# Optimization experiments

Hardware: AMD Instinct MI355X
Metric: run time of the kernel (lower is better)

## Reference

```python
import jax, jax.numpy as jnp
import numpy as np

# BiDAF-style co-attention with memory_len=2. Dropout is inference-mode identity.

def setup_inputs() -> dict:
    key = jax.random.key(0)
    k1, k2, k3, k4, k5 = jax.random.split(key, 5)
    d = 1024
    inp = jax.random.normal(k1, (8, 4096, d), dtype=jnp.float32)
    mem = jax.random.normal(k2, (8, 2, d), dtype=jnp.float32)
    w_input = jax.random.normal(k3, (d,), dtype=jnp.float32) * (1.0 / np.sqrt(d))
    w_memory = jax.random.normal(k4, (d,), dtype=jnp.float32) * (1.0 / np.sqrt(d))
    dot_scale = jax.random.uniform(k5, (d,), dtype=jnp.float32, minval=0.0, maxval=1.0 / np.sqrt(d))
    return {"input": inp, "memory": mem, "w_input": w_input, "w_memory": w_memory, "dot_scale": dot_scale}


def reference(input, memory, w_input, w_memory, dot_scale):
    # input: [b, L, d]; memory: [b, M=2, d]
    input_dot = jnp.einsum('bld,d->bl', input, w_input)[..., None]        # [b, L, 1]
    memory_dot = jnp.einsum('bmd,d->bm', memory, w_memory)[:, None, :]    # [b, 1, M]
    cross_dot = jnp.einsum('bld,bmd->blm', input * dot_scale, memory)     # [b, L, M]
    att = input_dot + memory_dot + cross_dot                              # [b, L, M]
    weight_one = jax.nn.softmax(att, axis=-1)                             # [b, L, M]
    output_one = jnp.einsum('blm,bmd->bld', weight_one, memory)           # [b, L, d]
    weight_two = jax.nn.softmax(jnp.max(att, axis=-1), axis=-1)           # [b, L]
    output_two = jnp.einsum('bl,bld->bd', weight_two, input)[:, None, :]  # [b, 1, d]
    return jnp.concatenate([input, output_one, input * output_one, output_two * output_one], axis=-1)
```

## Files before the change

### kernel.cpp

```cpp
#include <hip/hip_runtime.h>
#include <stdint.h>


#define BB 8
#define LL 4096
#define DD 1024
#define BPB 128
#define RPB 32
#define RPW 8

__global__ __launch_bounds__(256) void kP(const float* __restrict__ mem,
                                          const float* __restrict__ w_in,
                                          const float* __restrict__ w_mem,
                                          const float* __restrict__ ds,
                                          float* __restrict__ cvec,
                                          float* __restrict__ mdot) {
    int bm = blockIdx.x;
    int t  = threadIdx.x;
    const float* mrow = mem + bm * DD;
    float partial = 0.f;
#pragma unroll
    for (int j = 0; j < 4; ++j) {
        int d = t * 4 + j;
        float m = mrow[d];
        cvec[bm * DD + d] = fmaf(ds[d], m, w_in[d]);
        partial = fmaf(m, w_mem[d], partial);
    }
    __shared__ float red[4];
    for (int off = 32; off; off >>= 1) partial += __shfl_down(partial, off);
    if ((t & 63) == 0) red[t >> 6] = partial;
    __syncthreads();
    if (t == 0) mdot[bm] = red[0] + red[1] + red[2] + red[3];
}

__global__ __launch_bounds__(256) void kA(const float* __restrict__ input,
                                          const float* __restrict__ memory,
                                          const float* __restrict__ cvec,
                                          const float* __restrict__ mdot,
                                          float* __restrict__ att,
                                          float* __restrict__ pmax,
                                          float* __restrict__ pz,
                                          float* __restrict__ pacc,
                                          float* __restrict__ out) {
    int blk = blockIdx.x;
    int b = blk >> 7, chunk = blk & 127;
    int t = threadIdx.x;
    int wave = t >> 6, lane = t & 63;

    const float4* c0p = (const float4*)(cvec + (size_t)b * 2 * DD);
    const float4* c1p = c0p + DD / 4;
    const float4* m0p = (const float4*)(memory + (size_t)b * 2 * DD);
    const float4* m1p = m0p + DD / 4;
    float4 rc0[4], rc1[4], rm0[4], rm1[4], acc[4];
#pragma unroll
    for (int k = 0; k < 4; ++k) {
        rc0[k] = c0p[lane + 64 * k];
        rc1[k] = c1p[lane + 64 * k];
        rm0[k] = m0p[lane + 64 * k];
        rm1[k] = m1p[lane + 64 * k];
        acc[k] = make_float4(0.f, 0.f, 0.f, 0.f);
    }
    float md0 = mdot[b * 2], md1 = mdot[b * 2 + 1];
    float lmax = -1e30f, zsum = 0.f;

    int l0 = chunk * RPB + wave * RPW;
    for (int r = 0; r < RPW; ++r) {
        int l = l0 + r;
        const float4* row = (const float4*)(input + (size_t)(b * LL + l) * DD);
        float4 x[4];
#pragma unroll
        for (int k = 0; k < 4; ++k) x[k] = row[lane + 64 * k];

        float a0 = 0.f, a1 = 0.f;
#pragma unroll
        for (int k = 0; k < 4; ++k) {
            a0 = fmaf(x[k].x, rc0[k].x, a0); a0 = fmaf(x[k].y, rc0[k].y, a0);
            a0 = fmaf(x[k].z, rc0[k].z, a0); a0 = fmaf(x[k].w, rc0[k].w, a0);
            a1 = fmaf(x[k].x, rc1[k].x, a1); a1 = fmaf(x[k].y, rc1[k].y, a1);
            a1 = fmaf(x[k].z, rc1[k].z, a1); a1 = fmaf(x[k].w, rc1[k].w, a1);
        }
        for (int off = 32; off; off >>= 1) {
            a0 += __shfl_xor(a0, off);
            a1 += __shfl_xor(a1, off);
        }
        a0 += md0; a1 += md1;
        if (lane == 0) ((float2*)att)[(size_t)b * LL + l] = make_float2(a0, a1);

        float w0 = 1.f / (1.f + __expf(a1 - a0));
        float w1 = 1.f - w0;
        float ml = fmaxf(a0, a1);

        float e;
        if (ml > lmax) {
            float s = __expf(lmax - ml);
            zsum *= s;
#pragma unroll
            for (int k = 0; k < 4; ++k) {
                acc[k].x *= s; acc[k].y *= s; acc[k].z *= s; acc[k].w *= s;
            }
            lmax = ml;
            e = 1.f;
        } else {
            e = __expf(ml - lmax);
        }
        zsum += e;

        float* orow = out + (size_t)(b * LL + l) * (4 * DD);
#pragma unroll
        for (int k = 0; k < 4; ++k) {
            float4 o1;
            o1.x = fmaf(w0, rm0[k].x, w1 * rm1[k].x);
            o1.y = fmaf(w0, rm0[k].y, w1 * rm1[k].y);
            o1.z = fmaf(w0, rm0[k].z, w1 * rm1[k].z);
            o1.w = fmaf(w0, rm0[k].w, w1 * rm1[k].w);
            ((float4*)orow)[lane + 64 * k] = x[k];
            ((float4*)(orow + DD))[lane + 64 * k] = o1;
            ((float4*)(orow + 2 * DD))[lane + 64 * k] =
                make_float4(x[k].x * o1.x, x[k].y * o1.y,
                            x[k].z * o1.z, x[k].w * o1.w);
            acc[k].x = fmaf(e, x[k].x, acc[k].x);
            acc[k].y = fmaf(e, x[k].y, acc[k].y);
            acc[k].z = fmaf(e, x[k].z, acc[k].z);
            acc[k].w = fmaf(e, x[k].w, acc[k].w);
        }
    }

    __shared__ float swm[4], swz[4];
    __shared__ __align__(16) float sacc[DD];
    if (lane == 0) { swm[wave] = lmax; swz[wave] = zsum; }
    for (int j = t; j < DD; j += 256) sacc[j] = 0.f;
    __syncthreads();
    float bmax = fmaxf(fmaxf(swm[0], swm[1]), fmaxf(swm[2], swm[3]));
    float f = __expf(lmax - bmax);
#pragma unroll
    for (int k = 0; k < 4; ++k) {
        int idx = 4 * (lane + 64 * k);
        atomicAdd(&sacc[idx + 0], f * acc[k].x);
        atomicAdd(&sacc[idx + 1], f * acc[k].y);
        atomicAdd(&sacc[idx + 2], f * acc[k].z);
        atomicAdd(&sacc[idx + 3], f * acc[k].w);
    }
    __syncthreads();
    if (t == 0) {
        float bz = 0.f;
#pragma unroll
        for (int w = 0; w < 4; ++w) bz += swz[w] * __expf(swm[w] - bmax);
        pmax[blk] = bmax;
        pz[blk]   = bz;
    }
    ((float4*)(pacc + (size_t)blk * DD))[t] = ((const float4*)sacc)[t];
}

__global__ __launch_bounds__(256) void kB(const float* __restrict__ pmax,
                                          const float* __restrict__ pz,
                                          const float* __restrict__ pacc,
                                          float* __restrict__ out2) {
    int b = blockIdx.x, t = threadIdx.x;
    __shared__ float se[BPB];
    const float* pm = pmax + b * BPB;
    const float* pzb = pz + b * BPB;
    float m = -1e30f;
    for (int i = 0; i < BPB; ++i) m = fmaxf(m, pm[i]);
    if (t < BPB) se[t] = __expf(pm[t] - m);
    __syncthreads();
    float Z = 0.f;
    for (int i = 0; i < BPB; ++i) Z = fmaf(pzb[i], se[i], Z);
    float invZ = 1.f / Z;

    const float4* P = (const float4*)pacc + (size_t)b * BPB * (DD / 4);
    float4 a = make_float4(0.f, 0.f, 0.f, 0.f);
    for (int i = 0; i < BPB; ++i) {
        float e = se[i];
        float4 v = P[(size_t)i * 256 + t];
        a.x = fmaf(e, v.x, a.x);
        a.y = fmaf(e, v.y, a.y);
        a.z = fmaf(e, v.z, a.z);
        a.w = fmaf(e, v.w, a.w);
    }
    a.x *= invZ; a.y *= invZ; a.z *= invZ; a.w *= invZ;
    ((float4*)(out2 + (size_t)b * DD))[t] = a;
}

__global__ __launch_bounds__(256) void kE(const float* __restrict__ memory,
                                          const float* __restrict__ att,
                                          const float* __restrict__ out2,
                                          float* __restrict__ out) {
    int blk = blockIdx.x;
    int b = blk >> 8, chunk = blk & 255;
    int t = threadIdx.x;
    float4 m0 = ((const float4*)(memory + (size_t)b * 2 * DD))[t];
    float4 m1 = ((const float4*)(memory + (size_t)b * 2 * DD + DD))[t];
    float4 o2 = ((const float4*)(out2 + (size_t)b * DD))[t];
    const float2* attb = (const float2*)att + (size_t)b * LL + chunk * 16;
    for (int r = 0; r < 16; ++r) {
        float2 v = attb[r];
        float w0 = 1.f / (1.f + __expf(v.y - v.x));
        float w1 = 1.f - w0;
        float4 o1;
        o1.x = fmaf(w0, m0.x, w1 * m1.x);
        o1.y = fmaf(w0, m0.y, w1 * m1.y);
        o1.z = fmaf(w0, m0.z, w1 * m1.z);
        o1.w = fmaf(w0, m0.w, w1 * m1.w);
        float* orow = out + (size_t)(b * LL + chunk * 16 + r) * (4 * DD) + 3 * DD;
        ((float4*)orow)[t] = make_float4(o2.x * o1.x, o2.y * o1.y,
                                         o2.z * o1.z, o2.w * o1.w);
    }
}

extern "C" void kernel_launch(void* const* d_in, const int* in_sizes, int n_in,
                              void* d_out, int out_size, void* d_ws, size_t ws_size,
                              hipStream_t stream) {
    const float* input  = (const float*)d_in[0];
    const float* memory = (const float*)d_in[1];
    const float* w_in   = (const float*)d_in[2];
    const float* w_mem  = (const float*)d_in[3];
    const float* ds     = (const float*)d_in[4];
    float* out = (float*)d_out;

    float* ws    = (float*)d_ws;
    float* cvec  = ws;
    float* mdot  = ws + 16384;
    float* att   = ws + 16400;
    float* pmax  = ws + 81936;
    float* pz    = ws + 82960;
    float* out2  = ws + 83984;
    float* pacc  = ws + 92176;

    kP<<<16,   256, 0, stream>>>(memory, w_in, w_mem, ds, cvec, mdot);
    kA<<<1024, 256, 0, stream>>>(input, memory, cvec, mdot, att, pmax, pz, pacc, out);
    kB<<<BB,   256, 0, stream>>>(pmax, pz, pacc, out2);
    kE<<<2048, 256, 0, stream>>>(memory, att, out2, out);
}
```

Measured before the change: 691.6 us.

## Fold prep kernel into main pass, use nontemporal loads/stores, drop LDS atomics

```diff
diff --git a/kernel.cpp b/kernel.cpp
--- a/kernel.cpp
+++ b/kernel.cpp
@@ -5,39 +5,29 @@
 #define BB 8
 #define LL 4096
 #define DD 1024
+#define NBLK 1024
 #define BPB 128
 #define RPB 32
 #define RPW 8
 
-__global__ __launch_bounds__(256) void kP(const float* __restrict__ mem,
+typedef float f32x4 __attribute__((ext_vector_type(4)));
+
+static __device__ __forceinline__ f32x4 nt_load4(const float* p) {
+    return __builtin_nontemporal_load((const f32x4*)p);
+}
+static __device__ __forceinline__ void nt_store4(float* p, f32x4 v) {
+    __builtin_nontemporal_store(v, (f32x4*)p);
+}
+static __device__ __forceinline__ float hsum4(f32x4 v) {
+    return (v.x + v.y) + (v.z + v.w);
+}
+
+__global__ __launch_bounds__(256) void kA(const float* __restrict__ input,
+                                          const float* __restrict__ memory,
                                           const float* __restrict__ w_in,
                                           const float* __restrict__ w_mem,
                                           const float* __restrict__ ds,
-                                          float* __restrict__ cvec,
-                                          float* __restrict__ mdot) {
-    int bm = blockIdx.x;
-    int t  = threadIdx.x;
-    const float* mrow = mem + bm * DD;
-    float partial = 0.f;
-#pragma unroll
-    for (int j = 0; j < 4; ++j) {
-        int d = t * 4 + j;
-        float m = mrow[d];
-        cvec[bm * DD + d] = fmaf(ds[d], m, w_in[d]);
-        partial = fmaf(m, w_mem[d], partial);
-    }
-    __shared__ float red[4];
-    for (int off = 32; off; off >>= 1) partial += __shfl_down(partial, off);
-    if ((t & 63) == 0) red[t >> 6] = partial;
-    __syncthreads();
-    if (t == 0) mdot[bm] = red[0] + red[1] + red[2] + red[3];
-}
-
-__global__ __launch_bounds__(256) void kA(const float* __restrict__ input,
-                                          const float* __restrict__ memory,
-                                          const float* __restrict__ cvec,
-                                          const float* __restrict__ mdot,
-                                          float* __restrict__ att,
+                                          float* __restrict__ w0buf,
                                           float* __restrict__ pmax,
                                           float* __restrict__ pz,
                                           float* __restrict__ pacc,
@@ -47,47 +37,55 @@
     int t = threadIdx.x;
     int wave = t >> 6, lane = t & 63;
 
-    const float4* c0p = (const float4*)(cvec + (size_t)b * 2 * DD);
-    const float4* c1p = c0p + DD / 4;
-    const float4* m0p = (const float4*)(memory + (size_t)b * 2 * DD);
-    const float4* m1p = m0p + DD / 4;
-    float4 rc0[4], rc1[4], rm0[4], rm1[4], acc[4];
-#pragma unroll
-    for (int k = 0; k < 4; ++k) {
-        rc0[k] = c0p[lane + 64 * k];
-        rc1[k] = c1p[lane + 64 * k];
-        rm0[k] = m0p[lane + 64 * k];
-        rm1[k] = m1p[lane + 64 * k];
-        acc[k] = make_float4(0.f, 0.f, 0.f, 0.f);
-    }
-    float md0 = mdot[b * 2], md1 = mdot[b * 2 + 1];
+    f32x4 rc0[4], rc1[4], rm0[4], rm1[4], acc[4];
+    float md0 = 0.f, md1 = 0.f;
+    {
+        const float* m0p = memory + (size_t)b * 2 * DD;
+        const float* m1p = m0p + DD;
+#pragma unroll
+        for (int k = 0; k < 4; ++k) {
+            int i = 4 * (lane + 64 * k);
+            f32x4 m0 = *(const f32x4*)(m0p + i);
+            f32x4 m1 = *(const f32x4*)(m1p + i);
+            f32x4 wi = *(const f32x4*)(w_in + i);
+            f32x4 dv = *(const f32x4*)(ds + i);
+            f32x4 wm = *(const f32x4*)(w_mem + i);
+            rm0[k] = m0; rm1[k] = m1;
+            rc0[k] = wi + dv * m0;
+            rc1[k] = wi + dv * m1;
+            md0 += hsum4(m0 * wm);
+            md1 += hsum4(m1 * wm);
+            acc[k] = (f32x4)(0.f);
+        }
+        for (int off = 32; off; off >>= 1) {
+            md0 += __shfl_xor(md0, off);
+            md1 += __shfl_xor(md1, off);
+        }
+    }
+
     float lmax = -1e30f, zsum = 0.f;
-
     int l0 = chunk * RPB + wave * RPW;
+    const float* inb = input + (size_t)b * LL * DD;
     for (int r = 0; r < RPW; ++r) {
         int l = l0 + r;
-        const float4* row = (const float4*)(input + (size_t)(b * LL + l) * DD);
-        float4 x[4];
-#pragma unroll
-        for (int k = 0; k < 4; ++k) x[k] = row[lane + 64 * k];
-
-        float a0 = 0.f, a1 = 0.f;
-#pragma unroll
-        for (int k = 0; k < 4; ++k) {
-            a0 = fmaf(x[k].x, rc0[k].x, a0); a0 = fmaf(x[k].y, rc0[k].y, a0);
-            a0 = fmaf(x[k].z, rc0[k].z, a0); a0 = fmaf(x[k].w, rc0[k].w, a0);
-            a1 = fmaf(x[k].x, rc1[k].x, a1); a1 = fmaf(x[k].y, rc1[k].y, a1);
-            a1 = fmaf(x[k].z, rc1[k].z, a1); a1 = fmaf(x[k].w, rc1[k].w, a1);
-        }
+        const float* row = inb + (size_t)l * DD;
+        f32x4 x[4];
+#pragma unroll
+        for (int k = 0; k < 4; ++k) x[k] = nt_load4(row + 4 * (lane + 64 * k));
+
+        f32x4 s0 = x[0] * rc0[0], s1 = x[0] * rc1[0];
+#pragma unroll
+        for (int k = 1; k < 4; ++k) { s0 += x[k] * rc0[k]; s1 += x[k] * rc1[k]; }
+        float a0 = hsum4(s0), a1 = hsum4(s1);
         for (int off = 32; off; off >>= 1) {
             a0 += __shfl_xor(a0, off);
             a1 += __shfl_xor(a1, off);
         }
         a0 += md0; a1 += md1;
-        if (lane == 0) ((float2*)att)[(size_t)b * LL + l] = make_float2(a0, a1);
 
         float w0 = 1.f / (1.f + __expf(a1 - a0));
         float w1 = 1.f - w0;
+        if (lane == 0) w0buf[(size_t)b * LL + l] = w0;
         float ml = fmaxf(a0, a1);
 
         float e;
@@ -95,9 +93,7 @@
             float s = __expf(lmax - ml);
             zsum *= s;
 #pragma unroll
-            for (int k = 0; k < 4; ++k) {
-                acc[k].x *= s; acc[k].y *= s; acc[k].z *= s; acc[k].w *= s;
-            }
+            for (int k = 0; k < 4; ++k) acc[k] *= s;
             lmax = ml;
             e = 1.f;
         } else {
@@ -108,47 +104,38 @@
         float* orow = out + (size_t)(b * LL + l) * (4 * DD);
 #pragma unroll
         for (int k = 0; k < 4; ++k) {
-            float4 o1;
-            o1.x = fmaf(w0, rm0[k].x, w1 * rm1[k].x);
-            o1.y = fmaf(w0, rm0[k].y, w1 * rm1[k].y);
-            o1.z = fmaf(w0, rm0[k].z, w1 * rm1[k].z);
-            o1.w = fmaf(w0, rm0[k].w, w1 * rm1[k].w);
-            ((float4*)orow)[lane + 64 * k] = x[k];
-            ((float4*)(orow + DD))[lane + 64 * k] = o1;
-            ((float4*)(orow + 2 * DD))[lane + 64 * k] =
-                make_float4(x[k].x * o1.x, x[k].y * o1.y,
-                            x[k].z * o1.z, x[k].w * o1.w);
-            acc[k].x = fmaf(e, x[k].x, acc[k].x);
-            acc[k].y = fmaf(e, x[k].y, acc[k].y);
-            acc[k].z = fmaf(e, x[k].z, acc[k].z);
-            acc[k].w = fmaf(e, x[k].w, acc[k].w);
+            int i = 4 * (lane + 64 * k);
+            f32x4 o1 = w0 * rm0[k] + w1 * rm1[k];
+            nt_store4(orow + i, x[k]);
+            nt_store4(orow + DD + i, o1);
+            nt_store4(orow + 2 * DD + i, x[k] * o1);
+            acc[k] += e * x[k];
         }
     }
 
     __shared__ float swm[4], swz[4];
-    __shared__ __align__(16) float sacc[DD];
+    __shared__ __align__(16) float swacc[4][DD];
     if (lane == 0) { swm[wave] = lmax; swz[wave] = zsum; }
-    for (int j = t; j < DD; j += 256) sacc[j] = 0.f;
     __syncthreads();
     float bmax = fmaxf(fmaxf(swm[0], swm[1]), fmaxf(swm[2], swm[3]));
     float f = __expf(lmax - bmax);
 #pragma unroll
     for (int k = 0; k < 4; ++k) {
-        int idx = 4 * (lane + 64 * k);
-        atomicAdd(&sacc[idx + 0], f * acc[k].x);
-        atomicAdd(&sacc[idx + 1], f * acc[k].y);
-        atomicAdd(&sacc[idx + 2], f * acc[k].z);
-        atomicAdd(&sacc[idx + 3], f * acc[k].w);
+        *(f32x4*)(swacc[wave] + 4 * (lane + 64 * k)) = f * acc[k];
     }
     __syncthreads();
-    if (t == 0) {
-        float bz = 0.f;
-#pragma unroll
-        for (int w = 0; w < 4; ++w) bz += swz[w] * __expf(swm[w] - bmax);
-        pmax[blk] = bmax;
-        pz[blk]   = bz;
-    }
-    ((float4*)(pacc + (size_t)blk * DD))[t] = ((const float4*)sacc)[t];
+    {
+        f32x4 s = *(const f32x4*)(swacc[0] + 4 * t) + *(const f32x4*)(swacc[1] + 4 * t)
+                + *(const f32x4*)(swacc[2] + 4 * t) + *(const f32x4*)(swacc[3] + 4 * t);
+        *(f32x4*)(pacc + (size_t)blk * DD + 4 * t) = s;
+        if (t == 0) {
+            float bz = 0.f;
+#pragma unroll
+            for (int w = 0; w < 4; ++w) bz += swz[w] * __expf(swm[w] - bmax);
+            pmax[blk] = bmax;
+            pz[blk]   = bz;
+        }
+    }
 }
 
 __global__ __launch_bounds__(256) void kB(const float* __restrict__ pmax,
@@ -157,8 +144,8 @@
                                           float* __restrict__ out2) {
     int b = blockIdx.x, t = threadIdx.x;
     __shared__ float se[BPB];
-    const float* pm = pmax + b * BPB;
-    const float* pzb = pz + b * BPB;
+    const float* pm  = pmax + b * BPB;
+    const float* pzb = pz   + b * BPB;
     float m = -1e30f;
     for (int i = 0; i < BPB; ++i) m = fmaxf(m, pm[i]);
     if (t < BPB) se[t] = __expf(pm[t] - m);
@@ -167,43 +154,32 @@
     for (int i = 0; i < BPB; ++i) Z = fmaf(pzb[i], se[i], Z);
     float invZ = 1.f / Z;
 
-    const float4* P = (const float4*)pacc + (size_t)b * BPB * (DD / 4);
-    float4 a = make_float4(0.f, 0.f, 0.f, 0.f);
+    const float* P = pacc + (size_t)b * BPB * DD;
+    f32x4 a = (f32x4)(0.f);
     for (int i = 0; i < BPB; ++i) {
-        float e = se[i];
-        float4 v = P[(size_t)i * 256 + t];
-        a.x = fmaf(e, v.x, a.x);
-        a.y = fmaf(e, v.y, a.y);
-        a.z = fmaf(e, v.z, a.z);
-        a.w = fmaf(e, v.w, a.w);
-    }
-    a.x *= invZ; a.y *= invZ; a.z *= invZ; a.w *= invZ;
-    ((float4*)(out2 + (size_t)b * DD))[t] = a;
+        a += se[i] * *(const f32x4*)(P + (size_t)i * DD + 4 * t);
+    }
+    a *= invZ;
+    *(f32x4*)(out2 + (size_t)b * DD + 4 * t) = a;
 }
 
 __global__ __launch_bounds__(256) void kE(const float* __restrict__ memory,
-                                          const float* __restrict__ att,
+                                          const float* __restrict__ w0buf,
                                           const float* __restrict__ out2,
                                           float* __restrict__ out) {
     int blk = blockIdx.x;
     int b = blk >> 8, chunk = blk & 255;
     int t = threadIdx.x;
-    float4 m0 = ((const float4*)(memory + (size_t)b * 2 * DD))[t];
-    float4 m1 = ((const float4*)(memory + (size_t)b * 2 * DD + DD))[t];
-    float4 o2 = ((const float4*)(out2 + (size_t)b * DD))[t];
-    const float2* attb = (const float2*)att + (size_t)b * LL + chunk * 16;
+    f32x4 m0 = *(const f32x4*)(memory + (size_t)b * 2 * DD + 4 * t);
+    f32x4 m1 = *(const f32x4*)(memory + (size_t)b * 2 * DD + DD + 4 * t);
+    f32x4 o2 = *(const f32x4*)(out2 + (size_t)b * DD + 4 * t);
+    const float* w0b = w0buf + (size_t)b * LL + chunk * 16;
     for (int r = 0; r < 16; ++r) {
-        float2 v = attb[r];
-        float w0 = 1.f / (1.f + __expf(v.y - v.x));
+        float w0 = w0b[r];
         float w1 = 1.f - w0;
-        float4 o1;
-        o1.x = fmaf(w0, m0.x, w1 * m1.x);
-        o1.y = fmaf(w0, m0.y, w1 * m1.y);
-        o1.z = fmaf(w0, m0.z, w1 * m1.z);
-        o1.w = fmaf(w0, m0.w, w1 * m1.w);
+        f32x4 o1 = w0 * m0 + w1 * m1;
         float* orow = out + (size_t)(b * LL + chunk * 16 + r) * (4 * DD) + 3 * DD;
-        ((float4*)orow)[t] = make_float4(o2.x * o1.x, o2.y * o1.y,
-                                         o2.z * o1.z, o2.w * o1.w);
+        nt_store4(orow + 4 * t, o2 * o1);
     }
 }
 
@@ -218,16 +194,14 @@
     float* out = (float*)d_out;
 
     float* ws    = (float*)d_ws;
-    float* cvec  = ws;
-    float* mdot  = ws + 16384;
-    float* att   = ws + 16400;
-    float* pmax  = ws + 81936;
-    float* pz    = ws + 82960;
-    float* out2  = ws + 83984;
-    float* pacc  = ws + 92176;
-
-    kP<<<16,   256, 0, stream>>>(memory, w_in, w_mem, ds, cvec, mdot);
-    kA<<<1024, 256, 0, stream>>>(input, memory, cvec, mdot, att, pmax, pz, pacc, out);
+    float* w0buf = ws;
+    float* pmax  = ws + 32768;
+    float* pz    = ws + 33792;
+    float* out2  = ws + 34816;
+    float* pacc  = ws + 43008;
+
+    kA<<<NBLK, 256, 0, stream>>>(input, memory, w_in, w_mem, ds,
+                                 w0buf, pmax, pz, pacc, out);
     kB<<<BB,   256, 0, stream>>>(pmax, pz, pacc, out2);
-    kE<<<2048, 256, 0, stream>>>(memory, att, out2, out);
-}
+    kE<<<2048, 256, 0, stream>>>(memory, w0buf, out2, out);
+}
```

Measured after the change: 664.3 us. -3.9%, faster.
